# Kernel optimization log

Measured on AMD Instinct MI355X. Metric: run time of the kernel, lower is better.

Reference implementation:

```python
import jax, jax.numpy as jnp
import numpy as np

D = 1024
H = 16
HD = D // H  # 64
FF = 4 * D
EPS = 1e-5


def _xavier(key, shape):
    fan_in, fan_out = shape[1], shape[0]
    limit = float(np.sqrt(6.0 / (fan_in + fan_out)))
    return jax.random.uniform(key, shape, jnp.float32, -limit, limit)


def setup_inputs() -> dict:
    key = jax.random.key(0)
    ks = jax.random.split(key, 8)
    x = jax.random.normal(ks[0], (2, 2048, D), jnp.float32)
    return {
        "x": x,
        "w_qkv": _xavier(ks[1], (3 * D, D)),
        "b_qkv": jnp.zeros((3 * D,), jnp.float32),
        "w_out": _xavier(ks[2], (D, D)),
        "b_out": jnp.zeros((D,), jnp.float32),
        "w1": _xavier(ks[3], (FF, D)),
        "b1": jnp.zeros((FF,), jnp.float32),
        "w2": _xavier(ks[4], (D, FF)),
        "b2": jnp.zeros((D,), jnp.float32),
        "ln1_g": jnp.ones((D,), jnp.float32),
        "ln1_b": jnp.zeros((D,), jnp.float32),
        "ln2_g": jnp.ones((D,), jnp.float32),
        "ln2_b": jnp.zeros((D,), jnp.float32),
    }


def _layernorm(x, g, b):
    mu = jnp.mean(x, -1, keepdims=True)
    var = jnp.mean(jnp.square(x - mu), -1, keepdims=True)
    return (x - mu) * jax.lax.rsqrt(var + EPS) * g + b


def reference(x, w_qkv, b_qkv, w_out, b_out, w1, b1, w2, b2,
              ln1_g, ln1_b, ln2_g, ln2_b):
    B, S, _ = x.shape
    # pre-LN attention branch
    h = _layernorm(x, ln1_g, ln1_b)
    qkv = h @ w_qkv.T + b_qkv                      # [B,S,3D]
    qkv = qkv.reshape(B, S, H, 3 * HD).transpose(0, 2, 1, 3)  # [B,H,S,3hd]
    q, k, v = jnp.split(qkv, 3, axis=-1)
    scores = jnp.einsum('bhqd,bhkd->bhqk', q, k) / np.sqrt(HD)
    attn = jax.nn.softmax(scores, axis=-1)
    ctx = jnp.einsum('bhqk,bhkd->bhqd', attn, v)   # [B,H,S,hd]
    ctx = ctx.transpose(0, 2, 1, 3).reshape(B, S, D)
    x = x + (ctx @ w_out.T + b_out)
    # pre-LN MLP branch
    h = _layernorm(x, ln2_g, ln2_b)
    h = jax.nn.relu(h @ w1.T + b1)
    x = x + (h @ w2.T + b2)
    return x
```

## Files before the change

### kernel.cpp

```cpp
#include <hip/hip_runtime.h>
#include <hip/hip_bf16.h>

typedef __attribute__((ext_vector_type(8))) short bf16x8;
typedef __attribute__((ext_vector_type(4))) float f32x4;
typedef __attribute__((ext_vector_type(16))) float f32x16;
typedef __attribute__((ext_vector_type(4))) unsigned short u16x4;
typedef __attribute__((ext_vector_type(4))) unsigned int u32x4;
typedef unsigned short u16;

__device__ __forceinline__ u16 f2bf(float f) {
  unsigned u = __builtin_bit_cast(unsigned, f);
  u += 0x7fffu + ((u >> 16) & 1u);
  return (u16)(u >> 16);
}
__device__ __forceinline__ float bf2f(u16 u) {
  unsigned v = ((unsigned)u) << 16;
  return __builtin_bit_cast(float, v);
}
__device__ __forceinline__ unsigned cvt_pk_bf16(float lo, float hi) {
  unsigned r;
  asm("v_cvt_pk_bf16_f32 %0, %1, %2" : "=v"(r) : "v"(lo), "v"(hi));
  return r;
}
__device__ __forceinline__ float exp2_fast(float x) {
  float r;
  asm("v_exp_f32 %0, %1" : "=v"(r) : "v"(x));
  return r;
}

__device__ __forceinline__ void gl_lds16(const void* g, void* l) {
  __builtin_amdgcn_global_load_lds((const __attribute__((address_space(1))) void*)g,
                                   (__attribute__((address_space(3))) void*)l,
                                   16, 0, 0);
}

__device__ __forceinline__ void bar() {
  asm volatile("" ::: "memory");
  __builtin_amdgcn_s_barrier();
  asm volatile("" ::: "memory");
}

__global__ __launch_bounds__(256) void ln_cvt(const float* __restrict__ x,
                                              const float* __restrict__ g,
                                              const float* __restrict__ b,
                                              u16* __restrict__ out,
                                              const float* __restrict__ wa,
                                              const float* __restrict__ wb,
                                              const float* __restrict__ wc,
                                              const float* __restrict__ wd,
                                              u16* __restrict__ oa,
                                              u16* __restrict__ ob,
                                              u16* __restrict__ oc,
                                              u16* __restrict__ od) {
  __shared__ float red[8];
  const int t = threadIdx.x;
  if (blockIdx.x < 4096) {
    const int row = blockIdx.x;
    const int lane = t & 63, w = t >> 6;
    const float4 v = ((const float4*)(x + (size_t)row * 1024))[t];
    float s = v.x + v.y + v.z + v.w;
    float q = v.x * v.x + v.y * v.y + v.z * v.z + v.w * v.w;
#pragma unroll
    for (int off = 32; off; off >>= 1) {
      s += __shfl_down(s, off);
      q += __shfl_down(q, off);
    }
    if (lane == 0) { red[w] = s; red[4 + w] = q; }
    __syncthreads();
    s = red[0] + red[1] + red[2] + red[3];
    q = red[4] + red[5] + red[6] + red[7];
    const float mu = s * (1.f / 1024.f);
    const float var = q * (1.f / 1024.f) - mu * mu;
    const float rs = rsqrtf(var + 1e-5f);
    const float4 gv = ((const float4*)g)[t];
    const float4 bv = ((const float4*)b)[t];
    u16x4 o;
    o.x = f2bf((v.x - mu) * rs * gv.x + bv.x);
    o.y = f2bf((v.y - mu) * rs * gv.y + bv.y);
    o.z = f2bf((v.z - mu) * rs * gv.z + bv.z);
    o.w = f2bf((v.w - mu) * rs * gv.w + bv.w);
    ((u16x4*)(out + (size_t)row * 1024))[t] = o;
  } else {
    int i = (blockIdx.x - 4096) * 256 + t;
    const int stride = 2048 * 256;
    for (; i < 3145728; i += stride) {
      const float* src;
      u16* dst;
      int j;
      if (i < 786432) { src = wa; dst = oa; j = i; }
      else if (i < 1048576) { src = wb; dst = ob; j = i - 786432; }
      else if (i < 2097152) { src = wc; dst = oc; j = i - 1048576; }
      else { src = wd; dst = od; j = i - 2097152; }
      float4 v = ((const float4*)src)[j];
      u16x4 o;
      o.x = f2bf(v.x); o.y = f2bf(v.y); o.z = f2bf(v.z); o.w = f2bf(v.w);
      ((u16x4*)dst)[j] = o;
    }
  }
}

__global__ __launch_bounds__(256) void ln_k(const float* __restrict__ x,
                                            const float* __restrict__ g,
                                            const float* __restrict__ b,
                                            u16* __restrict__ out) {
  const int row = blockIdx.x;
  const int t = threadIdx.x;
  const int lane = t & 63, w = t >> 6;
  const float4 v = ((const float4*)(x + (size_t)row * 1024))[t];
  float s = v.x + v.y + v.z + v.w;
  float q = v.x * v.x + v.y * v.y + v.z * v.z + v.w * v.w;
#pragma unroll
  for (int off = 32; off; off >>= 1) {
    s += __shfl_down(s, off);
    q += __shfl_down(q, off);
  }
  __shared__ float red[8];
  if (lane == 0) { red[w] = s; red[4 + w] = q; }
  __syncthreads();
  s = red[0] + red[1] + red[2] + red[3];
  q = red[4] + red[5] + red[6] + red[7];
  const float mu = s * (1.f / 1024.f);
  const float var = q * (1.f / 1024.f) - mu * mu;
  const float rs = rsqrtf(var + 1e-5f);
  const float4 gv = ((const float4*)g)[t];
  const float4 bv = ((const float4*)b)[t];
  u16x4 o;
  o.x = f2bf((v.x - mu) * rs * gv.x + bv.x);
  o.y = f2bf((v.y - mu) * rs * gv.y + bv.y);
  o.z = f2bf((v.z - mu) * rs * gv.z + bv.z);
  o.w = f2bf((v.w - mu) * rs * gv.w + bv.w);
  ((u16x4*)(out + (size_t)row * 1024))[t] = o;
}

template <int BM, int BN, int BK, int TH, int WN, int MR, int NR, int EPI>
__global__ __launch_bounds__(TH, 2) void gemm_rot(const u16* __restrict__ A,
                                                  const u16* __restrict__ B,
                                                  const float* __restrict__ bias,
                                                  const float* __restrict__ res,
                                                  void* __restrict__ outp,
                                                  const int N, const int K) {
  constexpr int GPR = BK / 8;
  constexpr int KS = BK / 32;
  constexpr int AELEMS = BM * BK;
  constexpr int BELEMS = BN * BK;
  constexpr int NC = (BM + BN) * GPR / TH;
  static_assert((BM * GPR) % TH == 0 && ((BM + BN) * GPR) % TH == 0, "");
  __shared__ u16 lds[3][AELEMS + BELEMS];
  const int t = threadIdx.x;
  const int lane = t & 63, w = t >> 6;
  const int wm = w / WN, wn = w % WN;
  const int l15 = lane & 15, lhi = lane >> 4;
  const int nbx = gridDim.x;
  const int nwg = nbx * gridDim.y;
  const int orig = blockIdx.y * nbx + blockIdx.x;
  const int cpx = nwg >> 3;
  const int lid = (orig & 7) * cpx + (orig >> 3);
  const long bm = (long)(lid / nbx) * BM, bn = (long)(lid % nbx) * BN;
  const u16* Ab = A + bm * K;
  const u16* Bb = B + bn * K;
  const int nk = K / BK;

#define STAGE(kt_, bufi)                                                      \
  do {                                                                        \
    const long kk_ = (long)(kt_) * BK;                                        \
    _Pragma("unroll")                                                         \
    for (int j = 0; j < NC; ++j) {                                            \
      const int sj = j * TH + t;                                              \
      const u16* src_;                                                        \
      if ((j + 1) * TH <= BM * GPR) {                                         \
        const int row_ = sj / GPR, grp_ = sj % GPR;                           \
        const int g_ = (BK == 32) ? (grp_ ^ ((row_ >> 1) & 3))                \
                                  : (grp_ ^ (row_ & 7));                      \
        src_ = Ab + (size_t)row_ * K + kk_ + g_ * 8;                          \
      } else {                                                                \
        const int sb_ = sj - BM * GPR;                                        \
        const int row_ = sb_ / GPR, grp_ = sb_ % GPR;                         \
        const int g_ = (BK == 32) ? (grp_ ^ ((row_ >> 1) & 3))                \
                                  : (grp_ ^ (row_ & 7));                      \
        src_ = Bb + (size_t)row_ * K + kk_ + g_ * 8;                          \
      }                                                                       \
      gl_lds16(src_, &lds[bufi][(size_t)(j * TH + w * 64) * 8]);              \
    }                                                                         \
  } while (0)

  f32x4 acc[MR][NR] = {};
  STAGE(0, 0);
  STAGE(1, 1);
  for (int i = 0; i < nk; ++i) {
    if (i + 1 < nk) {
      if constexpr (NC == 3)      asm volatile("s_waitcnt vmcnt(3)" ::: "memory");
      else if constexpr (NC == 4) asm volatile("s_waitcnt vmcnt(4)" ::: "memory");
      else                        asm volatile("s_waitcnt vmcnt(6)" ::: "memory");
    } else {
      asm volatile("s_waitcnt vmcnt(0)" ::: "memory");
    }
    bar();
    if (i + 2 < nk) STAGE(i + 2, (i + 2) % 3);
    const u16* bufA = lds[i % 3];
    const u16* bufB = bufA + AELEMS;
    bf16x8 av[MR][KS], bv[NR][KS];
#pragma unroll
    for (int ii = 0; ii < MR; ++ii) {
      const int R = wm * (MR * 16) + ii * 16 + l15;
#pragma unroll
      for (int ks = 0; ks < KS; ++ks) {
        const int pos = (BK == 32) ? (lhi ^ ((R >> 1) & 3))
                                   : ((ks * 4 + lhi) ^ (R & 7));
        av[ii][ks] = *(const bf16x8*)&bufA[R * BK + (pos << 3)];
      }
    }
#pragma unroll
    for (int jj = 0; jj < NR; ++jj) {
      const int R = wn * (NR * 16) + jj * 16 + l15;
#pragma unroll
      for (int ks = 0; ks < KS; ++ks) {
        const int pos = (BK == 32) ? (lhi ^ ((R >> 1) & 3))
                                   : ((ks * 4 + lhi) ^ (R & 7));
        bv[jj][ks] = *(const bf16x8*)&bufB[R * BK + (pos << 3)];
      }
    }
    __builtin_amdgcn_s_setprio(1);
#pragma unroll
    for (int ii = 0; ii < MR; ++ii)
#pragma unroll
      for (int jj = 0; jj < NR; ++jj)
#pragma unroll
        for (int ks = 0; ks < KS; ++ks)
          acc[ii][jj] = __builtin_amdgcn_mfma_f32_16x16x32_bf16(av[ii][ks], bv[jj][ks],
                                                                acc[ii][jj], 0, 0, 0);
    __builtin_amdgcn_s_setprio(0);
  }
#undef STAGE
#pragma unroll
  for (int jj = 0; jj < NR; ++jj) {
    const long col = bn + wn * (NR * 16) + jj * 16 + l15;
    const float bj = bias[col];
#pragma unroll
    for (int ii = 0; ii < MR; ++ii) {
      const long row0 = bm + wm * (MR * 16) + ii * 16 + lhi * 4;
#pragma unroll
      for (int r = 0; r < 4; ++r) {
        const float v = acc[ii][jj][r] + bj;
        const long idx = (row0 + r) * N + col;
        if constexpr (EPI == 0) {
          ((u16*)outp)[idx] = f2bf(v);
        } else if constexpr (EPI == 1) {
          ((float*)outp)[idx] = v + res[idx];
        } else {
          ((u16*)outp)[idx] = f2bf(v > 0.f ? v : 0.f);
        }
      }
    }
  }
}

__global__ __launch_bounds__(256) void vtrans(const u16* __restrict__ qkv,
                                              u16* __restrict__ vt) {
  const int t = threadIdx.x;
  const int bh = blockIdx.y, b = bh >> 4, h = bh & 15;
  const int kvb = blockIdx.x * 64;
  __shared__ u16 tile[64][72];
  const u16* src = qkv + ((size_t)(b * 2048 + kvb)) * 3072 + h * 192 + 128;
#pragma unroll
  for (int rr = 0; rr < 2; ++rr) {
    const int e = rr * 2048 + t * 8;
    const int kv = e >> 6, d = e & 63;
    *(bf16x8*)&tile[kv][d] = *(const bf16x8*)(src + (size_t)kv * 3072 + d);
  }
  __syncthreads();
#pragma unroll
  for (int rr = 0; rr < 2; ++rr) {
    const int e = rr * 2048 + t * 8;
    const int d = e >> 6, kv = e & 63;
    bf16x8 o;
#pragma unroll
    for (int j = 0; j < 8; ++j) o[j] = (short)tile[kv + j][d];
    *(bf16x8*)(vt + ((size_t)bh * 64 + d) * 2048 + kvb + kv) = o;
  }
}

__global__ __launch_bounds__(256, 4) void attn_k(const u16* __restrict__ qkv,
                                                 const u16* __restrict__ vt,
                                                 u16* __restrict__ part0,
                                                 u16* __restrict__ part1,
                                                 float* __restrict__ lbuf) {
  __shared__ u16 kt[2][4096];
  __shared__ u16 vtl[2][4096];
  const int t = threadIdx.x;
  const int lane = t & 63, w = t >> 6;
  const int l31 = lane & 31, hl = lane >> 5;
  const int l7 = l31 & 7;
  const int bh = blockIdx.y, b = bh >> 4, h = bh & 15;
  const int qb = blockIdx.x * 128 + w * 32;
  const int sidx = blockIdx.z;
  const int kvbeg = sidx * 1024, kvend = kvbeg + 1024;

  const float qscale = 0.125f * 1.44269504f;
  const u16* qp = qkv + ((size_t)(b * 2048 + qb + l31)) * 3072 + h * 192;
  bf16x8 qf[4];
#pragma unroll
  for (int ds = 0; ds < 4; ++ds) {
    bf16x8 v = *(const bf16x8*)(qp + 16 * ds + 8 * hl);
#pragma unroll
    for (int j = 0; j < 8; ++j) v[j] = (short)f2bf(bf2f((u16)v[j]) * qscale);
    qf[ds] = v;
  }
  bf16x8 ones;
#pragma unroll
  for (int j = 0; j < 8; ++j) ones[j] = (short)0x3F80;

  const int srow = t >> 3, sgc = t & 7;
  const int sswz = (sgc ^ (srow & 7)) * 8;
  const u16* kg0 = qkv + ((size_t)(b * 2048 + srow)) * 3072 + h * 192 + 64 + sswz;
  const u16* vg0 = vt + (size_t)bh * 64 * 2048 + (size_t)srow * 2048 + sswz;

  f32x16 o0 = {}, o1 = {}, ol = {};

#define STAGE(bufi, kv0i)                                              \
  do {                                                                 \
    const u16* ks_ = kg0 + (size_t)(kv0i) * 3072;                      \
    const u16* vs_ = vg0 + (kv0i);                                     \
    gl_lds16(ks_, &kt[bufi][w * 512]);                                 \
    gl_lds16(ks_ + (size_t)32 * 3072, &kt[bufi][2048 + w * 512]);      \
    gl_lds16(vs_, &vtl[bufi][w * 512]);                                \
    gl_lds16(vs_ + (size_t)32 * 2048, &vtl[bufi][2048 + w * 512]);     \
  } while (0)

#define PACK(dst, SA, tl)                                                 \
  do {                                                                    \
    unsigned A0 = cvt_pk_bf16(SA[8 * tl + 0], SA[8 * tl + 1]);            \
    unsigned A1 = cvt_pk_bf16(SA[8 * tl + 2], SA[8 * tl + 3]);            \
    unsigned B0 = cvt_pk_bf16(SA[8 * tl + 4], SA[8 * tl + 5]);            \
    unsigned B1 = cvt_pk_bf16(SA[8 * tl + 6], SA[8 * tl + 7]);            \
    asm volatile("v_permlane32_swap_b32 %0, %1" : "+v"(A0), "+v"(B0));    \
    asm volatile("v_permlane32_swap_b32 %0, %1" : "+v"(A1), "+v"(B1));    \
    u32x4 pv_ = {A0, A1, B0, B1};                                         \
    dst = __builtin_bit_cast(bf16x8, pv_);                                \
  } while (0)

  int buf = 0;
  STAGE(0, kvbeg);
  for (int kv0 = kvbeg; kv0 < kvend; kv0 += 64) {
    asm volatile("s_waitcnt vmcnt(0)" ::: "memory");
    bar();
    if (kv0 + 64 < kvend) STAGE(buf ^ 1, kv0 + 64);
    f32x16 sa0 = {}, sa1 = {};
    __builtin_amdgcn_s_setprio(1);
#pragma unroll
    for (int ds = 0; ds < 4; ++ds) {
      const bf16x8 kf0 = *(const bf16x8*)&kt[buf][l31 * 64 + (((2 * ds + hl) ^ l7) << 3)];
      const bf16x8 kf1 = *(const bf16x8*)&kt[buf][(32 + l31) * 64 + (((2 * ds + hl) ^ l7) << 3)];
      sa0 = __builtin_amdgcn_mfma_f32_32x32x16_bf16(kf0, qf[ds], sa0, 0, 0, 0);
      sa1 = __builtin_amdgcn_mfma_f32_32x32x16_bf16(kf1, qf[ds], sa1, 0, 0, 0);
    }
    __builtin_amdgcn_s_setprio(0);
#pragma unroll
    for (int i = 0; i < 16; ++i) sa0[i] = exp2_fast(sa0[i]);
#pragma unroll
    for (int i = 0; i < 16; ++i) sa1[i] = exp2_fast(sa1[i]);
    bf16x8 pf0, pf1, pf2, pf3;
    PACK(pf0, sa0, 0);
    PACK(pf1, sa0, 1);
    PACK(pf2, sa1, 0);
    PACK(pf3, sa1, 1);
    __builtin_amdgcn_s_setprio(1);
#pragma unroll
    for (int t4i = 0; t4i < 4; ++t4i) {
      const bf16x8 vf0 = *(const bf16x8*)&vtl[buf][l31 * 64 + (((2 * t4i + hl) ^ l7) << 3)];
      const bf16x8 vf1 = *(const bf16x8*)&vtl[buf][(32 + l31) * 64 + (((2 * t4i + hl) ^ l7) << 3)];
      const bf16x8 pf = (t4i == 0) ? pf0 : (t4i == 1) ? pf1 : (t4i == 2) ? pf2 : pf3;
      o0 = __builtin_amdgcn_mfma_f32_32x32x16_bf16(vf0, pf, o0, 0, 0, 0);
      o1 = __builtin_amdgcn_mfma_f32_32x32x16_bf16(vf1, pf, o1, 0, 0, 0);
      ol = __builtin_amdgcn_mfma_f32_32x32x16_bf16(ones, pf, ol, 0, 0, 0);
    }
    __builtin_amdgcn_s_setprio(0);
    buf ^= 1;
  }
#undef STAGE
#undef PACK
  bar();
  if (lane < 32) {
    lbuf[(size_t)(sidx * 32 + bh) * 2048 + qb + l31] = ol[0];
  }
  u16* obase = (sidx == 0) ? part0 : part1;
  u16* ow = ((u16*)kt) + w * 2048;
#pragma unroll
  for (int g2 = 0; g2 < 4; ++g2) {
    uint2 v0, v1;
    v0.x = cvt_pk_bf16(o0[4 * g2 + 0], o0[4 * g2 + 1]);
    v0.y = cvt_pk_bf16(o0[4 * g2 + 2], o0[4 * g2 + 3]);
    v1.x = cvt_pk_bf16(o1[4 * g2 + 0], o1[4 * g2 + 1]);
    v1.y = cvt_pk_bf16(o1[4 * g2 + 2], o1[4 * g2 + 3]);
    *(uint2*)&ow[l31 * 64 + ((g2 ^ l7) << 3) + hl * 4] = v0;
    *(uint2*)&ow[l31 * 64 + (((4 + g2) ^ l7) << 3) + hl * 4] = v1;
  }
#pragma unroll
  for (int p = 0; p < 4; ++p) {
    const int q = 8 * p + (lane >> 3);
    const int gpos = lane & 7;
    const bf16x8 val = *(const bf16x8*)&ow[q * 64 + (gpos << 3)];
    const int gd = gpos ^ (q & 7);
    *(bf16x8*)(obase + ((size_t)(b * 2048 + qb + q)) * 1024 + h * 64 + gd * 8) = val;
  }
}

__global__ __launch_bounds__(256) void attn_merge(const u16* __restrict__ p1,
                                                  const float* __restrict__ lbuf,
                                                  u16* __restrict__ ctx) {
  const int c = blockIdx.x * 256 + threadIdx.x;
  const int row = c >> 7;
  const int b = row >> 11, q = row & 2047;
  const int h = (c >> 3) & 15;
  const int bh = b * 16 + h;
  const float l1 = lbuf[(size_t)bh * 2048 + q];
  const float l2 = lbuf[(size_t)(32 + bh) * 2048 + q];
  const float inv = 1.f / (l1 + l2);
  const bf16x8 v0 = ((const bf16x8*)ctx)[c];
  const bf16x8 v1 = ((const bf16x8*)p1)[c];
  float r[8];
#pragma unroll
  for (int j = 0; j < 8; ++j)
    r[j] = (bf2f((u16)v0[j]) + bf2f((u16)v1[j])) * inv;
  u32x4 ov = {cvt_pk_bf16(r[0], r[1]), cvt_pk_bf16(r[2], r[3]),
              cvt_pk_bf16(r[4], r[5]), cvt_pk_bf16(r[6], r[7])};
  ((u32x4*)ctx)[c] = ov;
}

extern "C" void kernel_launch(void* const* d_in, const int* in_sizes, int n_in,
                              void* d_out, int out_size, void* d_ws, size_t ws_size,
                              hipStream_t stream) {
  const float* x     = (const float*)d_in[0];
  const float* w_qkv = (const float*)d_in[1];
  const float* b_qkv = (const float*)d_in[2];
  const float* w_out = (const float*)d_in[3];
  const float* b_out = (const float*)d_in[4];
  const float* w1    = (const float*)d_in[5];
  const float* b1    = (const float*)d_in[6];
  const float* w2    = (const float*)d_in[7];
  const float* b2    = (const float*)d_in[8];
  const float* ln1g  = (const float*)d_in[9];
  const float* ln1b  = (const float*)d_in[10];
  const float* ln2g  = (const float*)d_in[11];
  const float* ln2b  = (const float*)d_in[12];
  float* out = (float*)d_out;

  u16* wqkv_b = (u16*)d_ws;
  u16* wout_b = wqkv_b + (size_t)3072 * 1024;
  u16* w1_b   = wout_b + (size_t)1024 * 1024;
  u16* w2_b   = w1_b + (size_t)4096 * 1024;
  u16* r1     = w2_b + (size_t)1024 * 4096;
  u16* r2     = r1 + (size_t)4096 * 1024;
  u16* qkvb   = r2;
  u16* vtb    = r2 + (size_t)4096 * 3072;
  float* x2   = (float*)(r2 + (size_t)4096 * 4096);
  u16* part1  = (u16*)x2;
  float* lbuf = (float*)(part1 + (size_t)4096 * 1024);

  ln_cvt<<<6144, 256, 0, stream>>>(x, ln1g, ln1b, r1,
                                   w_qkv, w_out, w1, w2,
                                   wqkv_b, wout_b, w1_b, w2_b);

  gemm_rot<128, 256, 32, 512, 4, 4, 4, 0><<<dim3(12, 32), 512, 0, stream>>>(
      r1, wqkv_b, b_qkv, nullptr, qkvb, 3072, 1024);
  vtrans<<<dim3(32, 32), 256, 0, stream>>>(qkvb, vtb);
  attn_k<<<dim3(16, 32, 2), 256, 0, stream>>>(qkvb, vtb, r1, part1, lbuf);
  attn_merge<<<2048, 256, 0, stream>>>(part1, lbuf, r1);
  gemm_rot<64, 128, 64, 256, 2, 2, 4, 1><<<dim3(8, 64), 256, 0, stream>>>(
      r1, wout_b, b_out, x, x2, 1024, 1024);
  ln_k<<<4096, 256, 0, stream>>>(x2, ln2g, ln2b, r1);
  gemm_rot<128, 256, 32, 512, 4, 4, 4, 2><<<dim3(16, 32), 512, 0, stream>>>(
      r1, w1_b, b1, nullptr, r2, 4096, 1024);
  gemm_rot<64, 128, 64, 256, 2, 2, 4, 1><<<dim3(8, 64), 256, 0, stream>>>(
      r2, w2_b, b2, x2, out, 1024, 4096);
}
```

Before: 213.3 us.

## Add 256x256 8-wave GEMM with XCD-aware block remap for QKV and FFN1

Introduces a new GEMM kernel with 256x256 output tiles, BK=64, 8 waves, an interleaved global-to-LDS staging schedule and XCD-aware workgroup remapping. It replaces the QKV and first FFN GEMMs. The attention kernel's block index is also remapped so related heads land on the same XCD. The larger tiles raise data reuse, but they also use 128KB of LDS and cut the grid to 192 or 256 blocks, which may underfill the 256 CUs. The epilogue writes bf16 one element at a time, uncoalesced.

```diff
diff --git a/kernel.cpp b/kernel.cpp
--- a/kernel.cpp
+++ b/kernel.cpp
@@ -132,6 +132,159 @@
   ((u16x4*)(out + (size_t)row * 1024))[t] = o;
 }
 
+template <int EPI>
+__global__ __launch_bounds__(512, 2) void gemm8(const u16* __restrict__ A,
+                                                const u16* __restrict__ B,
+                                                const float* __restrict__ bias,
+                                                void* __restrict__ outp,
+                                                const int N, const int K) {
+  __shared__ u16 lds[65536];
+  const int t = threadIdx.x;
+  const int lane = t & 63, w = t >> 6;
+  const int wm = w >> 2, wn = w & 3;
+  const int l15 = lane & 15, lhi = lane >> 4;
+  const int nbx = gridDim.x;
+  const int nwg = nbx * gridDim.y;
+  const int orig = blockIdx.y * nbx + blockIdx.x;
+  const int cpx = nwg >> 3;
+  const int lid = (orig & 7) * cpx + (orig >> 3);
+  const long bm = (long)(lid / nbx) * 256, bn = (long)(lid % nbx) * 256;
+  const u16* Ab = A + bm * K;
+  const u16* Bb = B + bn * K;
+  const int nt = K >> 6;
+  const int ni2 = nt >> 1;
+
+  const int srow0 = t >> 3, sg0 = (t & 7) ^ (srow0 & 7);
+  const int srow1 = 64 + srow0, sg1 = (t & 7) ^ (srow1 & 7);
+
+#define STAGE8(Mb, hf, kt_, dstb)                                             \
+  do {                                                                        \
+    const long kk_ = (long)(kt_) << 6;                                        \
+    gl_lds16(Mb + (size_t)((hf) * 128 + srow0) * K + kk_ + sg0 * 8,           \
+             &lds[(dstb) + w * 512]);                                         \
+    gl_lds16(Mb + (size_t)((hf) * 128 + srow1) * K + kk_ + sg1 * 8,           \
+             &lds[(dstb) + 4096 + w * 512]);                                  \
+  } while (0)
+
+#define LOADA(db, mi, fk0, fk1)                                               \
+  {                                                                           \
+    const int r_ = (mi) * 16 + l15;                                           \
+    const int b_ = ((db) * 2 + wm) * 8192 + r_ * 64;                          \
+    fk0 = *(const bf16x8*)&lds[b_ + ((lhi ^ (r_ & 7)) << 3)];                 \
+    fk1 = *(const bf16x8*)&lds[b_ + (((4 + lhi) ^ (r_ & 7)) << 3)];           \
+  }
+
+#define LOADB(db)                                                             \
+  _Pragma("unroll")                                                           \
+  for (int ni = 0; ni < 4; ++ni) {                                            \
+    const int R_ = wn * 64 + ni * 16 + l15;                                   \
+    const int b_ = 32768 + ((db) * 2 + (R_ >> 7)) * 8192 + (R_ & 127) * 64;   \
+    bq[ni][0] = *(const bf16x8*)&lds[b_ + ((lhi ^ (R_ & 7)) << 3)];           \
+    bq[ni][1] = *(const bf16x8*)&lds[b_ + (((4 + lhi) ^ (R_ & 7)) << 3)];     \
+  }
+
+#define MM(q, a0k0, a0k1, a1k0, a1k1)                                         \
+  __builtin_amdgcn_s_setprio(1);                                              \
+  _Pragma("unroll")                                                           \
+  for (int ni = 0; ni < 4; ++ni) {                                            \
+    acc[2 * (q)][ni] = __builtin_amdgcn_mfma_f32_16x16x32_bf16(               \
+        a0k0, bq[ni][0], acc[2 * (q)][ni], 0, 0, 0);                          \
+    acc[2 * (q)][ni] = __builtin_amdgcn_mfma_f32_16x16x32_bf16(               \
+        a0k1, bq[ni][1], acc[2 * (q)][ni], 0, 0, 0);                          \
+    acc[2 * (q) + 1][ni] = __builtin_amdgcn_mfma_f32_16x16x32_bf16(           \
+        a1k0, bq[ni][0], acc[2 * (q) + 1][ni], 0, 0, 0);                      \
+    acc[2 * (q) + 1][ni] = __builtin_amdgcn_mfma_f32_16x16x32_bf16(           \
+        a1k1, bq[ni][1], acc[2 * (q) + 1][ni], 0, 0, 0);                      \
+  }                                                                           \
+  __builtin_amdgcn_s_setprio(0);
+
+  f32x4 acc[8][4] = {};
+  STAGE8(Bb, 0, 0, 32768 + 0);
+  STAGE8(Bb, 1, 0, 32768 + 8192);
+  STAGE8(Ab, 0, 0, 0);
+  STAGE8(Ab, 1, 0, 8192);
+  STAGE8(Bb, 0, 1, 32768 + 16384);
+  STAGE8(Bb, 1, 1, 32768 + 24576);
+  asm volatile("s_waitcnt vmcnt(4)" ::: "memory");
+  bar();
+
+  for (int it = 0; it < ni2; ++it) {
+    const int t0 = 2 * it, t1 = 2 * it + 1;
+    const bool sN = (it + 1) < ni2;
+    bf16x8 bq[4][2];
+    bf16x8 a0, a1, a2, a3;
+    LOADA(0, 0, a0, a1) LOADA(0, 1, a2, a3) LOADB(0);
+    STAGE8(Ab, 0, t1, 16384);
+    bar();
+    MM(0, a0, a1, a2, a3)
+    bar();
+    LOADA(0, 2, a0, a1) LOADA(0, 3, a2, a3)
+    STAGE8(Ab, 1, t1, 24576);
+    if (sN) STAGE8(Bb, 0, t0 + 2, 32768 + 0);
+    bar();
+    MM(1, a0, a1, a2, a3)
+    bar();
+    LOADA(0, 4, a0, a1) LOADA(0, 5, a2, a3)
+    if (sN) STAGE8(Bb, 1, t0 + 2, 32768 + 8192);
+    bar();
+    MM(2, a0, a1, a2, a3)
+    bar();
+    LOADA(0, 6, a0, a1) LOADA(0, 7, a2, a3)
+    if (sN) asm volatile("s_waitcnt vmcnt(4)" ::: "memory");
+    else    asm volatile("s_waitcnt vmcnt(0)" ::: "memory");
+    bar();
+    MM(3, a0, a1, a2, a3)
+    bar();
+    LOADA(1, 0, a0, a1) LOADA(1, 1, a2, a3) LOADB(1);
+    if (sN) STAGE8(Ab, 0, t0 + 2, 0);
+    bar();
+    MM(0, a0, a1, a2, a3)
+    bar();
+    LOADA(1, 2, a0, a1) LOADA(1, 3, a2, a3)
+    if (sN) {
+      STAGE8(Ab, 1, t0 + 2, 8192);
+      STAGE8(Bb, 0, t1 + 2, 32768 + 16384);
+    }
+    bar();
+    MM(1, a0, a1, a2, a3)
+    bar();
+    LOADA(1, 4, a0, a1) LOADA(1, 5, a2, a3)
+    if (sN) STAGE8(Bb, 1, t1 + 2, 32768 + 24576);
+    bar();
+    MM(2, a0, a1, a2, a3)
+    bar();
+    LOADA(1, 6, a0, a1) LOADA(1, 7, a2, a3)
+    if (sN) asm volatile("s_waitcnt vmcnt(4)" ::: "memory");
+    else    asm volatile("s_waitcnt vmcnt(0)" ::: "memory");
+    bar();
+    MM(3, a0, a1, a2, a3)
+    bar();
+  }
+#undef STAGE8
+#undef LOADA
+#undef LOADB
+#undef MM
+#pragma unroll
+  for (int ni = 0; ni < 4; ++ni) {
+    const long col = bn + wn * 64 + ni * 16 + l15;
+    const float bj = bias[col];
+#pragma unroll
+    for (int mi = 0; mi < 8; ++mi) {
+      const long row0 = bm + wm * 128 + mi * 16 + lhi * 4;
+#pragma unroll
+      for (int r = 0; r < 4; ++r) {
+        const float v = acc[mi][ni][r] + bj;
+        const long idx = (row0 + r) * N + col;
+        if constexpr (EPI == 0) {
+          ((u16*)outp)[idx] = f2bf(v);
+        } else {
+          ((u16*)outp)[idx] = f2bf(v > 0.f ? v : 0.f);
+        }
+      }
+    }
+  }
+}
+
 template <int BM, int BN, int BK, int TH, int WN, int MR, int NR, int EPI>
 __global__ __launch_bounds__(TH, 2) void gemm_rot(const u16* __restrict__ A,
                                                   const u16* __restrict__ B,
@@ -290,9 +443,12 @@
   const int lane = t & 63, w = t >> 6;
   const int l31 = lane & 31, hl = lane >> 5;
   const int l7 = l31 & 7;
-  const int bh = blockIdx.y, b = bh >> 4, h = bh & 15;
-  const int qb = blockIdx.x * 128 + w * 32;
-  const int sidx = blockIdx.z;
+  const int lid = blockIdx.x + 16 * blockIdx.y + 512 * blockIdx.z;
+  const int bh = (lid & 7) * 4 + ((lid >> 3) & 3);
+  const int qblk = (lid >> 5) & 15;
+  const int sidx = lid >> 9;
+  const int b = bh >> 4, h = bh & 15;
+  const int qb = qblk * 128 + w * 32;
   const int kvbeg = sidx * 1024, kvend = kvbeg + 1024;
 
   const float qscale = 0.125f * 1.44269504f;
@@ -460,16 +616,14 @@
                                    w_qkv, w_out, w1, w2,
                                    wqkv_b, wout_b, w1_b, w2_b);
 
-  gemm_rot<128, 256, 32, 512, 4, 4, 4, 0><<<dim3(12, 32), 512, 0, stream>>>(
-      r1, wqkv_b, b_qkv, nullptr, qkvb, 3072, 1024);
+  gemm8<0><<<dim3(12, 16), 512, 0, stream>>>(r1, wqkv_b, b_qkv, qkvb, 3072, 1024);
   vtrans<<<dim3(32, 32), 256, 0, stream>>>(qkvb, vtb);
   attn_k<<<dim3(16, 32, 2), 256, 0, stream>>>(qkvb, vtb, r1, part1, lbuf);
   attn_merge<<<2048, 256, 0, stream>>>(part1, lbuf, r1);
   gemm_rot<64, 128, 64, 256, 2, 2, 4, 1><<<dim3(8, 64), 256, 0, stream>>>(
       r1, wout_b, b_out, x, x2, 1024, 1024);
   ln_k<<<4096, 256, 0, stream>>>(x2, ln2g, ln2b, r1);
-  gemm_rot<128, 256, 32, 512, 4, 4, 4, 2><<<dim3(16, 32), 512, 0, stream>>>(
-      r1, w1_b, b1, nullptr, r2, 4096, 1024);
+  gemm8<2><<<dim3(16, 16), 512, 0, stream>>>(r1, w1_b, b1, r2, 4096, 1024);
   gemm_rot<64, 128, 64, 256, 2, 2, 4, 1><<<dim3(8, 64), 256, 0, stream>>>(
       r2, w2_b, b2, x2, out, 1024, 4096);
 }
```

After: 212.1 us. About the same (-0.5%).
